# Kernel tuning notes

Hardware: AMD Instinct MI355X
Metric: run time of the kernel (lower is better)

The kernel has to match this reference:

```python
import jax, jax.numpy as jnp
import numpy as np

B, NQ, HW, D, H = 4, 100, 4096, 1024, 16
HD = D // H  # head dim = 64
EPS = 1e-5
NEG = -1e9


def layernorm(x, g, b):
    mu = jnp.mean(x, axis=-1, keepdims=True)
    var = jnp.mean(jnp.square(x - mu), axis=-1, keepdims=True)
    return (x - mu) * jax.lax.rsqrt(var + EPS) * g + b


def setup_inputs() -> dict:
    key = jax.random.key(0)
    ks = jax.random.split(key, 6)
    scale = 0.02
    return {
        "q": jax.random.normal(ks[0], (B, NQ, D), dtype=jnp.float32),
        "kv": jax.random.normal(ks[1], (B, HW, D), dtype=jnp.float32),
        "mask": jax.random.randint(ks[2], (B, NQ, HW), 0, 2, dtype=jnp.int32),
        "in_proj_w": scale * jax.random.normal(ks[3], (3 * D, D), dtype=jnp.float32),
        "in_proj_b": jnp.zeros((3 * D,), dtype=jnp.float32),
        "out_w": scale * jax.random.normal(ks[4], (D, D), dtype=jnp.float32),
        "out_b": jnp.zeros((D,), dtype=jnp.float32),
        "g_q": jnp.ones((D,), dtype=jnp.float32),
        "b_q": jnp.zeros((D,), dtype=jnp.float32),
        "g_kv": jnp.ones((D,), dtype=jnp.float32),
        "b_kv": jnp.zeros((D,), dtype=jnp.float32),
    }


def reference(q, kv, mask, in_proj_w, in_proj_b, out_w, out_b, g_q, b_q, g_kv, b_kv):
    qn = layernorm(q, g_q, b_q)      # [B,NQ,D]
    kvn = layernorm(kv, g_kv, b_kv)  # [B,HW,D]

    # nn.MultiheadAttention fused in-projection: rows [Wq; Wk; Wv]
    Wq, Wk, Wv = jnp.split(in_proj_w, 3, axis=0)
    bq, bk, bv = jnp.split(in_proj_b, 3, axis=0)
    qp = (qn @ Wq.T + bq).reshape(B, NQ, H, HD)
    kp = (kvn @ Wk.T + bk).reshape(B, HW, H, HD)
    vp = (kvn @ Wv.T + bv).reshape(B, HW, H, HD)

    scores = jnp.einsum("bqhd,bkhd->bhqk", qp, kp) / jnp.sqrt(jnp.float32(HD))

    # Per-query key mask; a query with an all-zero mask attends everywhere
    # (original code sets key_padding_mask=None when kpm.all()).
    allowed = mask.astype(bool)                                   # [B,NQ,HW]
    has_any = jnp.any(allowed, axis=-1, keepdims=True)
    eff = jnp.where(has_any, allowed, True)
    scores = jnp.where(eff[:, None, :, :], scores, NEG)

    attn = jax.nn.softmax(scores, axis=-1)                        # [B,H,NQ,HW]
    ctx = jnp.einsum("bhqk,bkhd->bqhd", attn, vp).reshape(B, NQ, D)
    return ctx @ out_w.T + out_b
```

## Files before the change

kernel.cpp:

```cpp
#include <hip/hip_runtime.h>
#include <math.h>
#include <stdint.h>

#define B_    4
#define NQ_   100
#define HW_   4096
#define D_    1024
#define H_    16
#define HD_   64
#define NCH_  4
#define KCH_  (HW_/NCH_)
#define NT_   (KCH_/128)
#define QT_   32
#define MP_   512

typedef __attribute__((ext_vector_type(8))) short short8;
typedef __attribute__((ext_vector_type(8))) unsigned short ushort8v;
typedef __attribute__((ext_vector_type(4))) float f32x4;

__device__ __forceinline__ unsigned short f2bf(float f) {
    unsigned int u = __float_as_uint(f);
    u += 0x7fffu + ((u >> 16) & 1u);
    return (unsigned short)(u >> 16);
}
__device__ __forceinline__ float bf2f(unsigned short h) {
    return __uint_as_float(((unsigned int)h) << 16);
}

__device__ __forceinline__ void gl2lds16(const void* g, void* l) {
    typedef __attribute__((address_space(1))) unsigned int gu32;
    typedef __attribute__((address_space(3))) unsigned int lu32;
    __builtin_amdgcn_global_load_lds(
        reinterpret_cast<gu32*>(reinterpret_cast<uintptr_t>(g)),
        reinterpret_cast<lu32*>(reinterpret_cast<uintptr_t>(l)),
        16, 0, 0);
}

#define VMCNT0() asm volatile("s_waitcnt vmcnt(0)" ::: "memory")
#define BARRIER() do { __builtin_amdgcn_s_barrier(); \
                       __builtin_amdgcn_sched_barrier(0); } while (0)

__global__ __launch_bounds__(256) void ln_bf16_kernel(
    const float* __restrict__ x, const float* __restrict__ g,
    const float* __restrict__ be, unsigned short* __restrict__ y, int real_rows)
{
    const int wv = threadIdx.x >> 6, lane = threadIdx.x & 63;
    const int row = blockIdx.x * 4 + wv;
    unsigned short* yr = y + (size_t)row * D_;
    if (row >= real_rows) {
        #pragma unroll
        for (int k = 0; k < 4; ++k)
            *reinterpret_cast<ushort4*>(yr + lane*4 + k*256) = make_ushort4(0,0,0,0);
        return;
    }
    const float* xr = x + (size_t)row * D_;
    float4 v[4];
    float s = 0.f, ss = 0.f;
    #pragma unroll
    for (int k = 0; k < 4; ++k) {
        v[k] = *reinterpret_cast<const float4*>(xr + lane*4 + k*256);
        s  += v[k].x + v[k].y + v[k].z + v[k].w;
        ss += v[k].x*v[k].x + v[k].y*v[k].y + v[k].z*v[k].z + v[k].w*v[k].w;
    }
    #pragma unroll
    for (int o = 1; o < 64; o <<= 1) {
        s  += __shfl_xor(s,  o);
        ss += __shfl_xor(ss, o);
    }
    const float mu = s * (1.0f / D_);
    const float rs = rsqrtf(ss * (1.0f / D_) - mu*mu + 1e-5f);
    #pragma unroll
    for (int k = 0; k < 4; ++k) {
        const float4 gg = *reinterpret_cast<const float4*>(g  + lane*4 + k*256);
        const float4 bb = *reinterpret_cast<const float4*>(be + lane*4 + k*256);
        ushort4 o;
        o.x = f2bf((v[k].x - mu) * rs * gg.x + bb.x);
        o.y = f2bf((v[k].y - mu) * rs * gg.y + bb.y);
        o.z = f2bf((v[k].z - mu) * rs * gg.z + bb.z);
        o.w = f2bf((v[k].w - mu) * rs * gg.w + bb.w);
        *reinterpret_cast<ushort4*>(yr + lane*4 + k*256) = o;
    }
}

__global__ __launch_bounds__(256) void wconv_kernel(
    const float* __restrict__ w, unsigned short* __restrict__ wb)
{
    const int i = blockIdx.x * 256 + threadIdx.x;
    const float4 v = reinterpret_cast<const float4*>(w)[i];
    ushort4 o;
    o.x = f2bf(v.x); o.y = f2bf(v.y); o.z = f2bf(v.z); o.w = f2bf(v.w);
    reinterpret_cast<ushort4*>(wb)[i] = o;
}

__global__ __launch_bounds__(256) void hilo_a_kernel(
    const float* __restrict__ x, unsigned short* __restrict__ y)
{
    const int row = blockIdx.x;
    const int tid = threadIdx.x;
    unsigned short* yr = y + (size_t)row * 3072;
    if (row >= B_*NQ_) {
        const ushort4 z = make_ushort4(0,0,0,0);
        reinterpret_cast<ushort4*>(yr)[tid]        = z;
        reinterpret_cast<ushort4*>(yr + 1024)[tid] = z;
        reinterpret_cast<ushort4*>(yr + 2048)[tid] = z;
        return;
    }
    const float4 v = reinterpret_cast<const float4*>(x + (size_t)row * D_)[tid];
    ushort4 hi, lo;
    hi.x = f2bf(v.x); hi.y = f2bf(v.y); hi.z = f2bf(v.z); hi.w = f2bf(v.w);
    lo.x = f2bf(v.x - bf2f(hi.x)); lo.y = f2bf(v.y - bf2f(hi.y));
    lo.z = f2bf(v.z - bf2f(hi.z)); lo.w = f2bf(v.w - bf2f(hi.w));
    reinterpret_cast<ushort4*>(yr)[tid]        = hi;
    reinterpret_cast<ushort4*>(yr + 1024)[tid] = lo;
    reinterpret_cast<ushort4*>(yr + 2048)[tid] = hi;
}

__global__ __launch_bounds__(256) void hilo_w_kernel(
    const float* __restrict__ w, unsigned short* __restrict__ y)
{
    const int row = blockIdx.x;
    const int tid = threadIdx.x;
    const float4 v = reinterpret_cast<const float4*>(w + (size_t)row * D_)[tid];
    ushort4 hi, lo;
    hi.x = f2bf(v.x); hi.y = f2bf(v.y); hi.z = f2bf(v.z); hi.w = f2bf(v.w);
    lo.x = f2bf(v.x - bf2f(hi.x)); lo.y = f2bf(v.y - bf2f(hi.y));
    lo.z = f2bf(v.z - bf2f(hi.z)); lo.w = f2bf(v.w - bf2f(hi.w));
    unsigned short* yr = y + (size_t)row * 3072;
    reinterpret_cast<ushort4*>(yr)[tid]        = hi;
    reinterpret_cast<ushort4*>(yr + 1024)[tid] = hi;
    reinterpret_cast<ushort4*>(yr + 2048)[tid] = lo;
}

__global__ __launch_bounds__(256) void mpack_kernel(
    const int* __restrict__ mask, unsigned int* __restrict__ mp)
{
    const int qrow = blockIdx.x;
    const int b = blockIdx.y;
    const int tid = threadIdx.x;
    unsigned int word = 0;
    if (qrow < NQ_ && tid < 128) {
        const int4* mr = reinterpret_cast<const int4*>(
            mask + ((size_t)(b*NQ_ + qrow))*HW_ + tid*32);
        #pragma unroll
        for (int j = 0; j < 8; ++j) {
            const int4 v = mr[j];
            word |= (v.x!=0 ? 1u:0u) << (4*j);
            word |= (v.y!=0 ? 1u:0u) << (4*j+1);
            word |= (v.z!=0 ? 1u:0u) << (4*j+2);
            word |= (v.w!=0 ? 1u:0u) << (4*j+3);
        }
    }
    const int wany = __any(word != 0) ? 1 : 0;
    __shared__ int red[4];
    if ((tid & 63) == 0) red[tid >> 6] = wany;
    __syncthreads();
    const int hasany = red[0] | red[1] | red[2] | red[3];
    if (tid < 128)
        mp[((size_t)(b*128 + qrow))*128 + tid] = hasany ? word : 0xFFFFFFFFu;
}

__global__ __launch_bounds__(512, 4) void gemm_kv_kernel(
    const unsigned short* __restrict__ A, const unsigned short* __restrict__ Wb,
    const float* __restrict__ bias, unsigned short* __restrict__ kp,
    unsigned short* __restrict__ vt)
{
    extern __shared__ __align__(16) unsigned short lds[];

    const int tid  = threadIdx.x;
    const int wave = tid >> 6;
    const int lane = tid & 63;
    const int lr   = lane & 15, quad = lane >> 4;
    const int wm2  = wave >> 2;
    const int wn4  = wave & 3;

    const int x  = blockIdx.x & 7;
    const int g  = blockIdx.x >> 3;
    const int bm = x*16 + (g >> 3);
    const int bn = g & 7;

    const int srow = tid >> 2;
    const int sswz = (srow & 3) ^ ((srow >> 2) & 3);
    const int scol = ((tid & 3) ^ sswz) * 8;
    const unsigned short* aSrc  = A  + (size_t)(bm*128 + srow)*D_ + scol;
    const unsigned short* bSrc0 = Wb + (size_t)(bn*256 + srow)*D_ + scol;
    const unsigned short* bSrc1 = bSrc0 + (size_t)128*D_;
    const int wdst = wave * 512;

    int aoff[4], boff[4];
    #pragma unroll
    for (int fm = 0; fm < 4; ++fm) {
        const int row = wm2*64 + fm*16 + lr;
        aoff[fm] = row*32 + (quad ^ (row & 3) ^ ((row >> 2) & 3))*8;
    }
    #pragma unroll
    for (int fn = 0; fn < 4; ++fn) {
        const int row = wn4*64 + fn*16 + lr;
        boff[fn] = 4096 + row*32 + (quad ^ (row & 3) ^ ((row >> 2) & 3))*8;
    }

    f32x4 acc[4][4];
    #pragma unroll
    for (int i = 0; i < 4; ++i)
        #pragma unroll
        for (int j = 0; j < 4; ++j)
            acc[i][j] = (f32x4){0.f, 0.f, 0.f, 0.f};

    gl2lds16(aSrc,  lds +        wdst);
    gl2lds16(bSrc0, lds + 4096 + wdst);
    gl2lds16(bSrc1, lds + 8192 + wdst);
    aSrc += 32; bSrc0 += 32; bSrc1 += 32;
    VMCNT0();
    BARRIER();

    int cur = 0;
    #pragma unroll 1
    for (int t = 0; t < 32; ++t) {
        const unsigned short* Sl = lds + cur*12288;
        unsigned short*       S2 = lds + (cur ^ 1)*12288;
        short8 afr[4], bfr[4];

        #pragma unroll
        for (int fm = 0; fm < 4; ++fm)
            afr[fm] = *reinterpret_cast<const short8*>(&Sl[aoff[fm]]);
        bfr[0] = *reinterpret_cast<const short8*>(&Sl[boff[0]]);
        bfr[1] = *reinterpret_cast<const short8*>(&Sl[boff[1]]);
        if (t < 31) {
            gl2lds16(aSrc,  S2 +        wdst);
            gl2lds16(bSrc0, S2 + 4096 + wdst);
        }
        __builtin_amdgcn_s_setprio(1);
        #pragma unroll
        for (int fm = 0; fm < 4; ++fm)
            #pragma unroll
            for (int fn = 0; fn < 2; ++fn)
                acc[fm][fn] = __builtin_amdgcn_mfma_f32_16x16x32_bf16(
                    afr[fm], bfr[fn], acc[fm][fn], 0, 0, 0);
        __builtin_amdgcn_s_setprio(0);

        bfr[2] = *reinterpret_cast<const short8*>(&Sl[boff[2]]);
        bfr[3] = *reinterpret_cast<const short8*>(&Sl[boff[3]]);
        if (t < 31) {
            gl2lds16(bSrc1, S2 + 8192 + wdst);
            aSrc += 32; bSrc0 += 32; bSrc1 += 32;
        }
        __builtin_amdgcn_s_setprio(1);
        #pragma unroll
        for (int fm = 0; fm < 4; ++fm)
            #pragma unroll
            for (int fn = 2; fn < 4; ++fn)
                acc[fm][fn] = __builtin_amdgcn_mfma_f32_16x16x32_bf16(
                    afr[fm], bfr[fn], acc[fm][fn], 0, 0, 0);
        __builtin_amdgcn_s_setprio(0);

        VMCNT0();
        BARRIER();
        cur ^= 1;
    }

    const int colbase = bn*256 + wn4*64 + lr;
    const int mbase   = bm*128 + wm2*64 + quad*4;
    if (bn < 4) {
        #pragma unroll
        for (int fn = 0; fn < 4; ++fn) {
            const int n = colbase + fn*16;
            const float bb = bias[n];
            #pragma unroll
            for (int fm = 0; fm < 4; ++fm) {
                unsigned short* Cp = kp + (size_t)(mbase + fm*16)*1024 + n;
                #pragma unroll
                for (int r = 0; r < 4; ++r)
                    Cp[(size_t)r * 1024] = f2bf(acc[fm][fn][r] + bb);
            }
        }
    } else {
        const int b = bm >> 5;
        const int key0 = mbase - b*4096;
        #pragma unroll
        for (int fn = 0; fn < 4; ++fn) {
            const int n = colbase + fn*16;
            const float bb = bias[n];
            unsigned short* vrow = vt + (size_t)(b*1024 + n - 1024) * HW_;
            #pragma unroll
            for (int fm = 0; fm < 4; ++fm) {
                ushort4 o;
                o.x = f2bf(acc[fm][fn][0] + bb);
                o.y = f2bf(acc[fm][fn][1] + bb);
                o.z = f2bf(acc[fm][fn][2] + bb);
                o.w = f2bf(acc[fm][fn][3] + bb);
                *reinterpret_cast<ushort4*>(vrow + key0 + fm*16) = o;
            }
        }
    }
}

__global__ __launch_bounds__(256) void gemm_splitk_kernel(
    const unsigned short* __restrict__ A, const unsigned short* __restrict__ W,
    float* __restrict__ P, int K, int KS)
{
    __shared__ __align__(16) unsigned short As[2048];
    __shared__ __align__(16) unsigned short Bs[2048];
    const int tid = threadIdx.x;
    const int wave = tid >> 6, lane = tid & 63;
    const int lr = lane & 15, quad = lane >> 4;
    const int bn = blockIdx.x, bm = blockIdx.y, sk = blockIdx.z;

    const int r0 = tid >> 2;
    const int xs = (r0 & 3) ^ ((r0 >> 2) & 3);
    const int kc = (tid & 3) ^ xs;
    const unsigned short* ap = A + (size_t)(bm*64 + r0)*K + sk*KS + kc*8;
    const unsigned short* bp = W + (size_t)(bn*64 + r0)*K + sk*KS + kc*8;
    unsigned short* asd = As + wave*512;
    unsigned short* bsd = Bs + wave*512;

    f32x4 acc[4];
    #pragma unroll
    for (int j = 0; j < 4; ++j) acc[j] = (f32x4){0.f,0.f,0.f,0.f};

    const int arow = wave*16 + lr;
    const int xa = (arow & 3) ^ ((arow >> 2) & 3);
    const int aoff = (arow*4 + (quad ^ xa))*8;
    int boff[4];
    #pragma unroll
    for (int j = 0; j < 4; ++j) {
        const int brow = j*16 + lr;
        const int xb = (brow & 3) ^ ((brow >> 2) & 3);
        boff[j] = (brow*4 + (quad ^ xb))*8;
    }

    const int nsteps = KS >> 5;
    for (int s = 0; s < nsteps; ++s) {
        gl2lds16(ap, asd); gl2lds16(bp, bsd);
        ap += 32; bp += 32;
        __syncthreads();
        const short8 af = *reinterpret_cast<const short8*>(&As[aoff]);
        short8 bf[4];
        #pragma unroll
        for (int j = 0; j < 4; ++j)
            bf[j] = *reinterpret_cast<const short8*>(&Bs[boff[j]]);
        #pragma unroll
        for (int j = 0; j < 4; ++j)
            acc[j] = __builtin_amdgcn_mfma_f32_16x16x32_bf16(af, bf[j], acc[j], 0, 0, 0);
        __syncthreads();
    }

    float* Pb = P + ((size_t)sk*MP_ + bm*64)*1024 + bn*64;
    const int m0 = wave*16 + quad*4;
    #pragma unroll
    for (int j = 0; j < 4; ++j)
        #pragma unroll
        for (int r = 0; r < 4; ++r)
            Pb[(size_t)(m0 + r)*1024 + j*16 + lr] = acc[j][r];
}

__global__ __launch_bounds__(256) void reduce_kernel(
    const float* __restrict__ P, const float* __restrict__ bias,
    float* __restrict__ Cout, int SK)
{
    const int i4 = blockIdx.x * 256 + threadIdx.x;
    const int c4 = i4 & 255;
    float4 s = reinterpret_cast<const float4*>(bias)[c4];
    for (int sk = 0; sk < SK; ++sk) {
        const float4 p = reinterpret_cast<const float4*>(P + (size_t)sk*MP_*1024)[i4];
        s.x += p.x; s.y += p.y; s.z += p.z; s.w += p.w;
    }
    reinterpret_cast<float4*>(Cout)[i4] = s;
}

__global__ __launch_bounds__(256) void flash_kernel(
    const float* __restrict__ qp, const unsigned short* __restrict__ kp,
    const unsigned short* __restrict__ vt, const unsigned int* __restrict__ mpack,
    float* __restrict__ partO, float* __restrict__ partL)
{
    __shared__ __align__(16) unsigned char smem[49152];
    unsigned short* Ks  = (unsigned short*)smem;
    unsigned short* Vts = (unsigned short*)(smem + 16384);
    unsigned short* Qs  = (unsigned short*)(smem + 32768);
    unsigned short* Ps  = (unsigned short*)(smem + 37376);
    unsigned int*   MWs = (unsigned int*)  (smem + 47616);
    float*          mlW = (float*)         (smem + 48128);
    float*          Om  = (float*)smem;

    const int tid = threadIdx.x;
    const int wave = tid >> 6, lane = tid & 63;
    const int lr = lane & 15, quad = lane >> 4;

    const int bid  = blockIdx.x;
    const int orig = (bid & 7) * 128 + (bid >> 3);
    const int qt   = orig & 3;
    const int rest = orig >> 2;
    const int h    = rest % H_;
    const int zz   = rest / H_;
    const int b    = zz / NCH_, ks = zz % NCH_;
    const int kb0 = ks * KCH_;

    {
        const int q = tid >> 3, dc = (tid & 7) * 8;
        const int qg = qt*QT_ + q;
        float4 v0 = make_float4(0.f,0.f,0.f,0.f), v1 = v0;
        if (qg < NQ_) {
            const float* src = qp + ((size_t)(b*NQ_ + qg))*D_ + h*HD_ + dc;
            v0 = *reinterpret_cast<const float4*>(src);
            v1 = *reinterpret_cast<const float4*>(src + 4);
        }
        ushort8v o;
        o[0]=f2bf(v0.x*0.125f); o[1]=f2bf(v0.y*0.125f);
        o[2]=f2bf(v0.z*0.125f); o[3]=f2bf(v0.w*0.125f);
        o[4]=f2bf(v1.x*0.125f); o[5]=f2bf(v1.y*0.125f);
        o[6]=f2bf(v1.z*0.125f); o[7]=f2bf(v1.w*0.125f);
        *reinterpret_cast<ushort8v*>(&Qs[q*72 + dc]) = o;
    }

    const unsigned short* kptr[4];
    const unsigned short* vptr[4];
    #pragma unroll
    for (int i = 0; i < 4; ++i) {
        const int s = i*256 + tid;
        const int key = s >> 3, jg = (s & 7) ^ (key & 7);
        kptr[i] = kp + ((size_t)(b*HW_) + kb0 + key)*1024 + h*HD_ + jg*8;
        const int d = s >> 4, js = s & 15, jg2 = js ^ (d & 15);
        vptr[i] = vt + ((size_t)(b*1024 + h*HD_ + d))*HW_ + kb0 + jg2*8;
    }

    int koff[2][2], voff[4];
    #pragma unroll
    for (int kj = 0; kj < 2; ++kj)
        #pragma unroll
        for (int ds = 0; ds < 2; ++ds) {
            const int key_l = wave*32 + kj*16 + lr;
            const int jg = ds*4 + quad;
            koff[kj][ds] = (key_l*8 + (jg ^ (key_l & 7))) * 8;
        }
    #pragma unroll
    for (int dj = 0; dj < 4; ++dj) {
        const int d_l = dj*16 + lr;
        const int jg = wave*4 + quad;
        voff[dj] = (d_l*16 + (jg ^ (d_l & 15))) * 8;
    }

    float lreg[8];
    #pragma unroll
    for (int i = 0; i < 8; ++i) lreg[i] = 0.f;
    f32x4 Ov[2][4];
    #pragma unroll
    for (int i = 0; i < 2; ++i)
        #pragma unroll
        for (int j = 0; j < 4; ++j)
            Ov[i][j] = (f32x4){0.f,0.f,0.f,0.f};

    for (int kt = 0; kt < NT_; ++kt) {
        __syncthreads();
        #pragma unroll
        for (int i = 0; i < 4; ++i) {
            gl2lds16(kptr[i], Ks  + (i*256 + wave*64)*8);
            gl2lds16(vptr[i], Vts + (i*256 + wave*64)*8);
            kptr[i] += 128*1024; vptr[i] += 128;
        }
        if (tid < 128) {
            const int mw = tid >> 5, mq = tid & 31;
            MWs[mw*32 + mq] = mpack[((size_t)(b*128 + qt*QT_ + mq))*128 +
                                    (ks*(KCH_/32) + kt*4 + mw)];
        }
        __syncthreads();

        f32x4 S[2][2];
        #pragma unroll
        for (int i = 0; i < 2; ++i)
            #pragma unroll
            for (int kj = 0; kj < 2; ++kj)
                S[i][kj] = (f32x4){0.f,0.f,0.f,0.f};
        #pragma unroll
        for (int ds = 0; ds < 2; ++ds) {
            short8 aq[2], bk[2];
            aq[0] = *reinterpret_cast<const short8*>(&Qs[(     lr)*72 + ds*32 + quad*8]);
            aq[1] = *reinterpret_cast<const short8*>(&Qs[(16 + lr)*72 + ds*32 + quad*8]);
            bk[0] = *reinterpret_cast<const short8*>(&Ks[koff[0][ds]]);
            bk[1] = *reinterpret_cast<const short8*>(&Ks[koff[1][ds]]);
            #pragma unroll
            for (int i = 0; i < 2; ++i)
                #pragma unroll
                for (int kj = 0; kj < 2; ++kj)
                    S[i][kj] = __builtin_amdgcn_mfma_f32_16x16x32_bf16(
                        aq[i], bk[kj], S[i][kj], 0, 0, 0);
        }

        #pragma unroll
        for (int i = 0; i < 2; ++i) {
            #pragma unroll
            for (int r = 0; r < 4; ++r) {
                const int q = i*16 + quad*4 + r;
                const unsigned int mw = MWs[wave*32 + q];
                const float p0 = ((mw >> lr) & 1u)        ? __expf(S[i][0][r]) : 0.f;
                const float p1 = ((mw >> (16 + lr)) & 1u) ? __expf(S[i][1][r]) : 0.f;
                lreg[i*4+r] += p0 + p1;
                const float p0n = __shfl_xor(p0, 1);
                const float p1n = __shfl_xor(p1, 1);
                if (!(lr & 1)) {
                    const unsigned int w0 = (unsigned)f2bf(p0) | ((unsigned)f2bf(p0n) << 16);
                    const unsigned int w1 = (unsigned)f2bf(p1) | ((unsigned)f2bf(p1n) << 16);
                    *reinterpret_cast<unsigned int*>(&Ps[wave*1280 + q*40 + lr])      = w0;
                    *reinterpret_cast<unsigned int*>(&Ps[wave*1280 + q*40 + 16 + lr]) = w1;
                }
            }
        }

        short8 pf[2], vf[4];
        #pragma unroll
        for (int i = 0; i < 2; ++i)
            pf[i] = *reinterpret_cast<const short8*>(&Ps[wave*1280 + (i*16+lr)*40 + quad*8]);
        #pragma unroll
        for (int dj = 0; dj < 4; ++dj)
            vf[dj] = *reinterpret_cast<const short8*>(&Vts[voff[dj]]);
        #pragma unroll
        for (int i = 0; i < 2; ++i)
            #pragma unroll
            for (int dj = 0; dj < 4; ++dj)
                Ov[i][dj] = __builtin_amdgcn_mfma_f32_16x16x32_bf16(
                    pf[i], vf[dj], Ov[i][dj], 0, 0, 0);
    }

    __syncthreads();
    #pragma unroll
    for (int i = 0; i < 2; ++i)
        #pragma unroll
        for (int r = 0; r < 4; ++r) {
            float l = lreg[i*4+r];
            #pragma unroll
            for (int o = 1; o < 16; o <<= 1) l += __shfl_xor(l, o);
            if (lr == 0) mlW[wave*32 + i*16 + quad*4 + r] = l;
        }
    #pragma unroll
    for (int i = 0; i < 2; ++i)
        #pragma unroll
        for (int dj = 0; dj < 4; ++dj)
            #pragma unroll
            for (int r = 0; r < 4; ++r) {
                const int q = i*16 + quad*4 + r;
                Om[wave*2112 + q*66 + dj*16 + lr] = Ov[i][dj][r];
            }
    __syncthreads();
    {
        const int q = tid >> 3, dc = (tid & 7) * 8;
        float L = 0.f;
        #pragma unroll
        for (int w = 0; w < 4; ++w) L += mlW[w*32 + q];
        float os[8] = {};
        #pragma unroll
        for (int w = 0; w < 4; ++w)
            #pragma unroll
            for (int j = 0; j < 8; ++j)
                os[j] += Om[w*2112 + q*66 + dc + j];
        const size_t pr = (((size_t)(b*H_ + h))*NCH_ + ks)*128 + qt*QT_ + q;
        *reinterpret_cast<float4*>(&partO[pr*HD_ + dc])     = make_float4(os[0],os[1],os[2],os[3]);
        *reinterpret_cast<float4*>(&partO[pr*HD_ + dc + 4]) = make_float4(os[4],os[5],os[6],os[7]);
        if ((tid & 7) == 0) partL[pr] = L;
    }
}

__global__ __launch_bounds__(64) void combine_kernel(
    const float* __restrict__ partO, const float* __restrict__ partL,
    float* __restrict__ ctx)
{
    const int d = threadIdx.x;
    const int qi = blockIdx.x, h = blockIdx.y, b = blockIdx.z;
    const size_t base = ((size_t)(b*H_ + h)) * NCH_ * 128;
    float L = 0.f, O = 0.f;
    #pragma unroll
    for (int i = 0; i < NCH_; ++i) {
        const size_t r = base + i*128 + qi;
        L += partL[r];
        O += partO[r*HD_ + d];
    }
    ctx[((size_t)(b*NQ_ + qi))*D_ + h*HD_ + d] = O / L;
}

extern "C" void kernel_launch(void* const* d_in, const int* in_sizes, int n_in,
                              void* d_out, int out_size, void* d_ws, size_t ws_size,
                              hipStream_t stream)
{
    const float* q     = (const float*)d_in[0];
    const float* kv    = (const float*)d_in[1];
    const int*   mask  = (const int*)  d_in[2];
    const float* in_w  = (const float*)d_in[3];
    const float* in_b  = (const float*)d_in[4];
    const float* out_w = (const float*)d_in[5];
    const float* out_b = (const float*)d_in[6];
    const float* g_q   = (const float*)d_in[7];
    const float* b_q   = (const float*)d_in[8];
    const float* g_kv  = (const float*)d_in[9];
    const float* b_kv  = (const float*)d_in[10];
    float* out = (float*)d_out;

    char* ws = (char*)d_ws;
    float*          qp       = (float*)         (ws + 0);
    unsigned int*   mpackp   = (unsigned int*)  (ws + 1638400);
    unsigned short* wfull_bf = (unsigned short*)(ws + 1900544);
    unsigned short* qn_bf    = (unsigned short*)(ws + 8192000);
    unsigned short* ctx_cat  = (unsigned short*)(ws + 9240576);
    unsigned short* wout_cat = (unsigned short*)(ws + 12386304);
    float*          P        = (float*)         (ws + 18677760);
    float*          ctx      = (float*)         (ws + 35454976);
    float*          partL    = (float*)         (ws + 37093376);
    float*          partO    = (float*)         (ws + 37355520);
    unsigned short* kvn_bf   = (unsigned short*)(ws + 54132736);
    unsigned short* kp       = (unsigned short*)(ws + 87687168);
    unsigned short* vt       = (unsigned short*)(ws + 121241600);

    static bool attr_set = false;
    if (!attr_set) {
        hipFuncSetAttribute(reinterpret_cast<const void*>(gemm_kv_kernel),
                            hipFuncAttributeMaxDynamicSharedMemorySize, 49152);
        attr_set = true;
    }

    mpack_kernel<<<dim3(128, B_), 256, 0, stream>>>(mask, mpackp);
    wconv_kernel<<<3*D_*D_/4/256, 256, 0, stream>>>(in_w, wfull_bf);
    ln_bf16_kernel<<<B_*HW_/4, 256, 0, stream>>>(kv, g_kv, b_kv, kvn_bf, B_*HW_);
    ln_bf16_kernel<<<MP_/4, 256, 0, stream>>>(q, g_q, b_q, qn_bf, B_*NQ_);

    gemm_splitk_kernel<<<dim3(D_/64, MP_/64, 8), 256, 0, stream>>>(
        qn_bf, wfull_bf, P, D_, 128);
    reduce_kernel<<<B_*NQ_*D_/4/256, 256, 0, stream>>>(P, in_b, qp, 8);

    gemm_kv_kernel<<<dim3(1024), 512, 49152, stream>>>(
        kvn_bf, wfull_bf + (size_t)D_*D_, in_b + D_, kp, vt);

    flash_kernel<<<dim3(4*H_*B_*NCH_), 256, 0, stream>>>(
        qp, kp, vt, mpackp, partO, partL);
    combine_kernel<<<dim3(NQ_, H_, B_), 64, 0, stream>>>(partO, partL, ctx);

    hilo_a_kernel<<<MP_, 256, 0, stream>>>(ctx, ctx_cat);
    hilo_w_kernel<<<D_, 256, 0, stream>>>(out_w, wout_cat);
    gemm_splitk_kernel<<<dim3(D_/64, MP_/64, 8), 256, 0, stream>>>(
        ctx_cat, wout_cat, P, 3*D_, 384);
    reduce_kernel<<<B_*NQ_*D_/4/256, 256, 0, stream>>>(P, out_b, out, 8);
}
```

Baseline: 300.3 us.

## Fuse prep kernels into one launch, merge combine into hilo split, halve KV chunks

Five preprocessing kernels (KV and Q layernorm, in-proj weight conversion, out-proj hi/lo split, mask packing) become one prep kernel that dispatches on block index. The split-K combine of flash partials is folded into the hi/lo activation split, which drops one launch and the fp32 ctx round trip. The flash kernel now splits keys into 2 chunks instead of 4, with the block-index swizzle generalized to match. This halves the partial traffic but also halves the number of flash blocks, which lowers parallelism on a large GPU.

Result: faster. 283.9 us (-5.4%).

```diff
diff --git a/kernel.cpp b/kernel.cpp
--- a/kernel.cpp
+++ b/kernel.cpp
@@ -8,7 +8,7 @@
 #define D_    1024
 #define H_    16
 #define HD_   64
-#define NCH_  4
+#define NCH_  2
 #define KCH_  (HW_/NCH_)
 #define NT_   (KCH_/128)
 #define QT_   32
@@ -40,12 +40,11 @@
 #define BARRIER() do { __builtin_amdgcn_s_barrier(); \
                        __builtin_amdgcn_sched_barrier(0); } while (0)
 
-__global__ __launch_bounds__(256) void ln_bf16_kernel(
+__device__ __forceinline__ void ln_row(
     const float* __restrict__ x, const float* __restrict__ g,
-    const float* __restrict__ be, unsigned short* __restrict__ y, int real_rows)
-{
-    const int wv = threadIdx.x >> 6, lane = threadIdx.x & 63;
-    const int row = blockIdx.x * 4 + wv;
+    const float* __restrict__ be, unsigned short* __restrict__ y,
+    int row, int real_rows, int lane)
+{
     unsigned short* yr = y + (size_t)row * D_;
     if (row >= real_rows) {
         #pragma unroll
@@ -82,81 +81,62 @@
     }
 }
 
-__global__ __launch_bounds__(256) void wconv_kernel(
-    const float* __restrict__ w, unsigned short* __restrict__ wb)
-{
-    const int i = blockIdx.x * 256 + threadIdx.x;
-    const float4 v = reinterpret_cast<const float4*>(w)[i];
-    ushort4 o;
-    o.x = f2bf(v.x); o.y = f2bf(v.y); o.z = f2bf(v.z); o.w = f2bf(v.w);
-    reinterpret_cast<ushort4*>(wb)[i] = o;
-}
-
-__global__ __launch_bounds__(256) void hilo_a_kernel(
-    const float* __restrict__ x, unsigned short* __restrict__ y)
-{
-    const int row = blockIdx.x;
-    const int tid = threadIdx.x;
-    unsigned short* yr = y + (size_t)row * 3072;
-    if (row >= B_*NQ_) {
-        const ushort4 z = make_ushort4(0,0,0,0);
-        reinterpret_cast<ushort4*>(yr)[tid]        = z;
-        reinterpret_cast<ushort4*>(yr + 1024)[tid] = z;
-        reinterpret_cast<ushort4*>(yr + 2048)[tid] = z;
-        return;
-    }
-    const float4 v = reinterpret_cast<const float4*>(x + (size_t)row * D_)[tid];
-    ushort4 hi, lo;
-    hi.x = f2bf(v.x); hi.y = f2bf(v.y); hi.z = f2bf(v.z); hi.w = f2bf(v.w);
-    lo.x = f2bf(v.x - bf2f(hi.x)); lo.y = f2bf(v.y - bf2f(hi.y));
-    lo.z = f2bf(v.z - bf2f(hi.z)); lo.w = f2bf(v.w - bf2f(hi.w));
-    reinterpret_cast<ushort4*>(yr)[tid]        = hi;
-    reinterpret_cast<ushort4*>(yr + 1024)[tid] = lo;
-    reinterpret_cast<ushort4*>(yr + 2048)[tid] = hi;
-}
-
-__global__ __launch_bounds__(256) void hilo_w_kernel(
-    const float* __restrict__ w, unsigned short* __restrict__ y)
-{
-    const int row = blockIdx.x;
-    const int tid = threadIdx.x;
-    const float4 v = reinterpret_cast<const float4*>(w + (size_t)row * D_)[tid];
-    ushort4 hi, lo;
-    hi.x = f2bf(v.x); hi.y = f2bf(v.y); hi.z = f2bf(v.z); hi.w = f2bf(v.w);
-    lo.x = f2bf(v.x - bf2f(hi.x)); lo.y = f2bf(v.y - bf2f(hi.y));
-    lo.z = f2bf(v.z - bf2f(hi.z)); lo.w = f2bf(v.w - bf2f(hi.w));
-    unsigned short* yr = y + (size_t)row * 3072;
-    reinterpret_cast<ushort4*>(yr)[tid]        = hi;
-    reinterpret_cast<ushort4*>(yr + 1024)[tid] = hi;
-    reinterpret_cast<ushort4*>(yr + 2048)[tid] = lo;
-}
-
-__global__ __launch_bounds__(256) void mpack_kernel(
-    const int* __restrict__ mask, unsigned int* __restrict__ mp)
-{
-    const int qrow = blockIdx.x;
-    const int b = blockIdx.y;
-    const int tid = threadIdx.x;
-    unsigned int word = 0;
-    if (qrow < NQ_ && tid < 128) {
-        const int4* mr = reinterpret_cast<const int4*>(
-            mask + ((size_t)(b*NQ_ + qrow))*HW_ + tid*32);
-        #pragma unroll
-        for (int j = 0; j < 8; ++j) {
-            const int4 v = mr[j];
-            word |= (v.x!=0 ? 1u:0u) << (4*j);
-            word |= (v.y!=0 ? 1u:0u) << (4*j+1);
-            word |= (v.z!=0 ? 1u:0u) << (4*j+2);
-            word |= (v.w!=0 ? 1u:0u) << (4*j+3);
-        }
-    }
-    const int wany = __any(word != 0) ? 1 : 0;
+__global__ __launch_bounds__(256) void prep_kernel(
+    const float* __restrict__ kv,   const float* __restrict__ g_kv,
+    const float* __restrict__ b_kv, unsigned short* __restrict__ kvn,
+    const float* __restrict__ qf,   const float* __restrict__ g_q,
+    const float* __restrict__ b_q,  unsigned short* __restrict__ qn,
+    const float* __restrict__ in_w, unsigned short* __restrict__ wfull,
+    const float* __restrict__ out_w, unsigned short* __restrict__ wout,
+    const int* __restrict__ mask,   unsigned int* __restrict__ mp)
+{
     __shared__ int red[4];
-    if ((tid & 63) == 0) red[tid >> 6] = wany;
-    __syncthreads();
-    const int hasany = red[0] | red[1] | red[2] | red[3];
-    if (tid < 128)
-        mp[((size_t)(b*128 + qrow))*128 + tid] = hasany ? word : 0xFFFFFFFFu;
+    const int bid = blockIdx.x, tid = threadIdx.x;
+
+    if (bid < 4096) {
+        ln_row(kv, g_kv, b_kv, kvn, bid*4 + (tid >> 6), B_*HW_, tid & 63);
+    } else if (bid < 7168) {
+        const int i = (bid - 4096)*256 + tid;
+        const float4 v = reinterpret_cast<const float4*>(in_w)[i];
+        ushort4 o;
+        o.x = f2bf(v.x); o.y = f2bf(v.y); o.z = f2bf(v.z); o.w = f2bf(v.w);
+        reinterpret_cast<ushort4*>(wfull)[i] = o;
+    } else if (bid < 8192) {
+        const int row = bid - 7168;
+        const float4 v = reinterpret_cast<const float4*>(out_w + (size_t)row * D_)[tid];
+        ushort4 hi, lo;
+        hi.x = f2bf(v.x); hi.y = f2bf(v.y); hi.z = f2bf(v.z); hi.w = f2bf(v.w);
+        lo.x = f2bf(v.x - bf2f(hi.x)); lo.y = f2bf(v.y - bf2f(hi.y));
+        lo.z = f2bf(v.z - bf2f(hi.z)); lo.w = f2bf(v.w - bf2f(hi.w));
+        unsigned short* yr = wout + (size_t)row * 3072;
+        reinterpret_cast<ushort4*>(yr)[tid]        = hi;
+        reinterpret_cast<ushort4*>(yr + 1024)[tid] = hi;
+        reinterpret_cast<ushort4*>(yr + 2048)[tid] = lo;
+    } else if (bid < 8704) {
+        const int mblk = bid - 8192;
+        const int qrow = mblk & 127, mb = mblk >> 7;
+        unsigned int word = 0;
+        if (qrow < NQ_ && tid < 128) {
+            const int4* mr = reinterpret_cast<const int4*>(
+                mask + ((size_t)(mb*NQ_ + qrow))*HW_ + tid*32);
+            #pragma unroll
+            for (int j = 0; j < 8; ++j) {
+                const int4 v = mr[j];
+                word |= (v.x!=0 ? 1u:0u) << (4*j);
+                word |= (v.y!=0 ? 1u:0u) << (4*j+1);
+                word |= (v.z!=0 ? 1u:0u) << (4*j+2);
+                word |= (v.w!=0 ? 1u:0u) << (4*j+3);
+            }
+        }
+        const int wany = __any(word != 0) ? 1 : 0;
+        if ((tid & 63) == 0) red[tid >> 6] = wany;
+        __syncthreads();
+        const int hasany = red[0] | red[1] | red[2] | red[3];
+        if (tid < 128)
+            mp[((size_t)(mb*128 + qrow))*128 + tid] = hasany ? word : 0xFFFFFFFFu;
+    } else {
+        ln_row(qf, g_q, b_q, qn, (bid - 8704)*4 + (tid >> 6), B_*NQ_, tid & 63);
+    }
 }
 
 __global__ __launch_bounds__(512, 4) void gemm_kv_kernel(
@@ -384,8 +364,9 @@
     const int wave = tid >> 6, lane = tid & 63;
     const int lr = lane & 15, quad = lane >> 4;
 
+    const int CPX  = (4*H_*B_*NCH_) / 8;
     const int bid  = blockIdx.x;
-    const int orig = (bid & 7) * 128 + (bid >> 3);
+    const int orig = (bid & 7) * CPX + (bid >> 3);
     const int qt   = orig & 3;
     const int rest = orig >> 2;
     const int h    = rest % H_;
@@ -556,21 +537,40 @@
     }
 }
 
-__global__ __launch_bounds__(64) void combine_kernel(
+__global__ __launch_bounds__(256) void hilo_a_kernel(
     const float* __restrict__ partO, const float* __restrict__ partL,
-    float* __restrict__ ctx)
-{
-    const int d = threadIdx.x;
-    const int qi = blockIdx.x, h = blockIdx.y, b = blockIdx.z;
-    const size_t base = ((size_t)(b*H_ + h)) * NCH_ * 128;
-    float L = 0.f, O = 0.f;
+    unsigned short* __restrict__ y)
+{
+    const int row = blockIdx.x;
+    const int tid = threadIdx.x;
+    unsigned short* yr = y + (size_t)row * 3072;
+    if (row >= B_*NQ_) {
+        const ushort4 z = make_ushort4(0,0,0,0);
+        reinterpret_cast<ushort4*>(yr)[tid]        = z;
+        reinterpret_cast<ushort4*>(yr + 1024)[tid] = z;
+        reinterpret_cast<ushort4*>(yr + 2048)[tid] = z;
+        return;
+    }
+    const int b = row / NQ_, qi = row % NQ_;
+    const int h = tid >> 4, d4 = (tid & 15) * 4;
+    float4 O = make_float4(0.f, 0.f, 0.f, 0.f);
+    float L = 0.f;
     #pragma unroll
     for (int i = 0; i < NCH_; ++i) {
-        const size_t r = base + i*128 + qi;
-        L += partL[r];
-        O += partO[r*HD_ + d];
-    }
-    ctx[((size_t)(b*NQ_ + qi))*D_ + h*HD_ + d] = O / L;
+        const size_t pr = (((size_t)(b*H_ + h))*NCH_ + i)*128 + qi;
+        const float4 p = *reinterpret_cast<const float4*>(partO + pr*HD_ + d4);
+        O.x += p.x; O.y += p.y; O.z += p.z; O.w += p.w;
+        L += partL[pr];
+    }
+    const float ri = 1.0f / L;
+    const float4 v = make_float4(O.x*ri, O.y*ri, O.z*ri, O.w*ri);
+    ushort4 hi, lo;
+    hi.x = f2bf(v.x); hi.y = f2bf(v.y); hi.z = f2bf(v.z); hi.w = f2bf(v.w);
+    lo.x = f2bf(v.x - bf2f(hi.x)); lo.y = f2bf(v.y - bf2f(hi.y));
+    lo.z = f2bf(v.z - bf2f(hi.z)); lo.w = f2bf(v.w - bf2f(hi.w));
+    reinterpret_cast<ushort4*>(yr)[tid]        = hi;
+    reinterpret_cast<ushort4*>(yr + 1024)[tid] = lo;
+    reinterpret_cast<ushort4*>(yr + 2048)[tid] = hi;
 }
 
 extern "C" void kernel_launch(void* const* d_in, const int* in_sizes, int n_in,
@@ -598,7 +598,6 @@
     unsigned short* ctx_cat  = (unsigned short*)(ws + 9240576);
     unsigned short* wout_cat = (unsigned short*)(ws + 12386304);
     float*          P        = (float*)         (ws + 18677760);
-    float*          ctx      = (float*)         (ws + 35454976);
     float*          partL    = (float*)         (ws + 37093376);
     float*          partO    = (float*)         (ws + 37355520);
     unsigned short* kvn_bf   = (unsigned short*)(ws + 54132736);
@@ -612,10 +611,12 @@
         attr_set = true;
     }
 
-    mpack_kernel<<<dim3(128, B_), 256, 0, stream>>>(mask, mpackp);
-    wconv_kernel<<<3*D_*D_/4/256, 256, 0, stream>>>(in_w, wfull_bf);
-    ln_bf16_kernel<<<B_*HW_/4, 256, 0, stream>>>(kv, g_kv, b_kv, kvn_bf, B_*HW_);
-    ln_bf16_kernel<<<MP_/4, 256, 0, stream>>>(q, g_q, b_q, qn_bf, B_*NQ_);
+    prep_kernel<<<8832, 256, 0, stream>>>(
+        kv, g_kv, b_kv, kvn_bf,
+        q,  g_q,  b_q,  qn_bf,
+        in_w, wfull_bf,
+        out_w, wout_cat,
+        mask, mpackp);
 
     gemm_splitk_kernel<<<dim3(D_/64, MP_/64, 8), 256, 0, stream>>>(
         qn_bf, wfull_bf, P, D_, 128);
@@ -626,10 +627,8 @@
 
     flash_kernel<<<dim3(4*H_*B_*NCH_), 256, 0, stream>>>(
         qp, kp, vt, mpackp, partO, partL);
-    combine_kernel<<<dim3(NQ_, H_, B_), 64, 0, stream>>>(partO, partL, ctx);
-
-    hilo_a_kernel<<<MP_, 256, 0, stream>>>(ctx, ctx_cat);
-    hilo_w_kernel<<<D_, 256, 0, stream>>>(out_w, wout_cat);
+
+    hilo_a_kernel<<<MP_, 256, 0, stream>>>(partO, partL, ctx_cat);
     gemm_splitk_kernel<<<dim3(D_/64, MP_/64, 8), 256, 0, stream>>>(
         ctx_cat, wout_cat, P, 3*D_, 384);
     reduce_kernel<<<B_*NQ_*D_/4/256, 256, 0, stream>>>(P, out_b, out, 8);
```
